# Performance work log

Measured on AMD Instinct MI355X. Metric: run time of the kernel, lower is better.

Reference implementation:

```python
import jax, jax.numpy as jnp
import numpy as np

B, T, C_IN = 64, 2048, 44
D = 512                      # d_model
DC = D // 2 + D // 2 + D // 4  # combined_dim = 640
RED = DC // 4                # SE reduction dim = 160
EPS = 1e-5


def setup_inputs() -> dict:
    key = jax.random.key(0)
    ks = iter(jax.random.split(key, 32))
    def w(shape, scale=None):
        s = scale if scale is not None else 1.0 / np.sqrt(shape[0])
        return jax.random.uniform(next(ks), shape, jnp.float32, -s, s)
    return {
        "x": jax.random.normal(next(ks), (B, T, C_IN), jnp.float32),
        # grouped projections (weights stored [in, out])
        "hw1": w((14, D // 2)), "hb1": w((D // 2,), 1.0 / np.sqrt(14)),
        "hw2": w((D // 2, D // 2)), "hb2": w((D // 2,)),
        "lw1": w((22, D // 2)), "lb1": w((D // 2,), 1.0 / np.sqrt(22)),
        "lw2": w((D // 2, D // 2)), "lb2": w((D // 2,)),
        "ew1": w((8, D // 4)), "eb1": w((D // 4,), 1.0 / np.sqrt(8)),
        "ew2": w((D // 4, D // 4)), "eb2": w((D // 4,)),
        # SE block (no bias)
        "se_w1": w((DC, RED)), "se_w2": w((RED, DC)),
        # SymmetryGate
        "gw": w((DC, DC)), "gb": w((DC,)),
        "pw": w((DC, DC)), "pb": w((DC,)),
        "ln_w": jnp.ones((DC,), jnp.float32), "ln_b": jnp.zeros((DC,), jnp.float32),
        # output proj + GroupNorm(8, D)
        "ow": w((DC, D)), "ob": w((DC,))[:D] if DC >= D else w((D,)),
        "gn_w": jnp.ones((D,), jnp.float32), "gn_b": jnp.zeros((D,), jnp.float32),
    }


def reference(x, hw1, hb1, hw2, hb2, lw1, lb1, lw2, lb2, ew1, eb1, ew2, eb2,
              se_w1, se_w2, gw, gb, pw, pb, ln_w, ln_b, ow, ob, gn_w, gn_b):
    silu = jax.nn.silu
    # grouped projections on channel slices (scale=2 -> 14/22/8)
    z_h = silu(x[..., :14] @ hw1 + hb1) @ hw2 + hb2        # [B,T,D/2]
    z_l = silu(x[..., 14:36] @ lw1 + lb1) @ lw2 + lb2      # [B,T,D/2]
    z_e = silu(x[..., 36:44] @ ew1 + eb1) @ ew2 + eb2      # [B,T,D/4]
    z = jnp.concatenate([z_h, z_l, z_e], axis=-1)          # [B,T,DC]
    # SE block: global time-average pooling then channel gating
    y_avg = z.mean(axis=1)                                  # [B,DC]
    se = jax.nn.sigmoid(jax.nn.relu(y_avg @ se_w1) @ se_w2) # [B,DC]
    z_se = z * se[:, None, :]
    # SymmetryGate (GLU + LayerNorm)
    g = jax.nn.sigmoid(z_se @ gw + gb)
    p = z_se @ pw + pb
    h = g * p + (1.0 - g) * z_se
    mu = h.mean(axis=-1, keepdims=True)
    var = h.var(axis=-1, keepdims=True)
    h = (h - mu) * jax.lax.rsqrt(var + EPS) * ln_w + ln_b
    # output projection
    out = h @ ow + ob                                       # [B,T,D]
    # GroupNorm(8, D) over channels (PyTorch normalizes per (group, T))
    G = 8
    og = out.reshape(B, T, G, D // G)
    m = og.mean(axis=(1, 3), keepdims=True)
    v = og.var(axis=(1, 3), keepdims=True)
    og = (og - m) * jax.lax.rsqrt(v + EPS)
    out = og.reshape(B, T, D) * gn_w + gn_b
    return out
```

## Files before the change

### kernel.cpp

```cpp
#include <hip/hip_runtime.h>
#include <hip/hip_bf16.h>
#include <cstdint>

#define B_   64
#define T_   2048
#define CIN  44
#define D_   512
#define DCC  640
#define REDD 160
#define BT   131072
#define EPSV 1e-5f

typedef __attribute__((ext_vector_type(8))) short short8;
typedef __attribute__((ext_vector_type(4))) float f32x4;

#define MFMA16(a,b,c) __builtin_amdgcn_mfma_f32_16x16x32_bf16(a,b,c,0,0,0)

__device__ __forceinline__ float bf2f(unsigned short u) {
    union { unsigned int i; float f; } v; v.i = ((unsigned int)u) << 16; return v.f;
}
__device__ __forceinline__ unsigned short f2bf(float f) {
    union { float f; unsigned int i; } v; v.f = f;
    unsigned int r = v.i + 0x7FFFu + ((v.i >> 16) & 1u);
    return (unsigned short)(r >> 16);
}

__global__ void kprep(const float* __restrict__ hw1, const float* __restrict__ lw1, const float* __restrict__ ew1,
                      const float* __restrict__ hb1, const float* __restrict__ lb1, const float* __restrict__ eb1,
                      const float* __restrict__ hw2, const float* __restrict__ lw2, const float* __restrict__ ew2,
                      const float* __restrict__ hb2, const float* __restrict__ lb2, const float* __restrict__ eb2,
                      const float* __restrict__ gw,  const float* __restrict__ pw,  const float* __restrict__ ow,
                      unsigned short* __restrict__ w1T, float* __restrict__ b1,
                      unsigned short* __restrict__ w2T, float* __restrict__ b2,
                      unsigned short* __restrict__ gwT, unsigned short* __restrict__ pwT,
                      unsigned short* __restrict__ owT)
{
    int tid = blockIdx.x * blockDim.x + threadIdx.x;
    int nth = gridDim.x * blockDim.x;
    for (int i = tid; i < 640 * 640; i += nth) {
        int c  = i / 40960, r = i - c * 40960;
        int kb = r / 2048;  int r2 = r - kb * 2048;
        int t  = r2 >> 9;   int l8 = r2 & 511;
        int lane = l8 >> 3, j = l8 & 7;
        int lid = lane & 15, quad = lane >> 4;
        int n = c * 64 + t * 16 + lid;
        int k = kb * 32 + quad * 8 + j;
        gwT[i] = f2bf(gw[(size_t)k * 640 + n]);
        pwT[i] = f2bf(pw[(size_t)k * 640 + n]);
    }
    for (int i = tid; i < 512 * 640; i += nth) {
        int c  = i / 40960, r = i - c * 40960;
        int kb = r / 2048;  int r2 = r - kb * 2048;
        int t  = r2 >> 9;   int l8 = r2 & 511;
        int lane = l8 >> 3, j = l8 & 7;
        int lid = lane & 15, quad = lane >> 4;
        int n = c * 64 + t * 16 + lid;
        int k = kb * 32 + quad * 8 + j;
        owT[i] = f2bf(ow[(size_t)k * 512 + n]);
    }
    for (int i = tid; i < 640 * 256; i += nth) {
        int c  = i / 16384, r = i - c * 16384;
        int kb = r / 2048;  int r2 = r - kb * 2048;
        int t  = r2 >> 9;   int l8 = r2 & 511;
        int lane = l8 >> 3, j = l8 & 7;
        int lid = lane & 15, quad = lane >> 4;
        int n = c * 64 + t * 16 + lid;
        int k = kb * 32 + quad * 8 + j;
        float v;
        if (n < 256)      v = hw2[k * 256 + n];
        else if (n < 512) v = lw2[k * 256 + (n - 256)];
        else              v = (k < 128) ? ew2[k * 128 + (n - 512)] : 0.0f;
        w2T[i] = f2bf(v);
    }
    for (int i = tid; i < 640 * 32; i += nth) {
        int ct = i >> 9;  int l8 = i & 511;
        int lane = l8 >> 3, j = l8 & 7;
        int lid = lane & 15, quad = lane >> 4;
        int n = ct * 16 + lid;
        int k = quad * 8 + j;
        float v = 0.0f;
        if (n < 256)      { if (k < 14) v = hw1[k * 256 + n]; }
        else if (n < 512) { if (k < 22) v = lw1[k * 256 + (n - 256)]; }
        else              { if (k < 8)  v = ew1[k * 128 + (n - 512)]; }
        w1T[i] = f2bf(v);
    }
    for (int i = tid; i < 640; i += nth) {
        b1[i] = (i < 256) ? hb1[i] : ((i < 512) ? lb1[i - 256] : eb1[i - 512]);
        b2[i] = (i < 256) ? hb2[i] : ((i < 512) ? lb2[i - 256] : eb2[i - 512]);
    }
}

#define ZSTEP(KB, CUR, NXT) { \
    const int kk = (KB) * 32; \
    short8 ah0 = *(const short8*)&su[(0*16 + lid) * 648 + kk + quad * 8]; \
    short8 ah1 = *(const short8*)&su[(1*16 + lid) * 648 + kk + quad * 8]; \
    short8 ah2 = *(const short8*)&su[(2*16 + lid) * 648 + kk + quad * 8]; \
    short8 ah3 = *(const short8*)&su[(3*16 + lid) * 648 + kk + quad * 8]; \
    short8 al0 = *(const short8*)&su[(0*16 + lid) * 648 + 256 + kk + quad * 8]; \
    short8 al1 = *(const short8*)&su[(1*16 + lid) * 648 + 256 + kk + quad * 8]; \
    short8 al2 = *(const short8*)&su[(2*16 + lid) * 648 + 256 + kk + quad * 8]; \
    short8 al3 = *(const short8*)&su[(3*16 + lid) * 648 + 256 + kk + quad * 8]; \
    if ((KB) + 1 < 8) { \
        NXT[0] = *(const short8*)(w2T + off[0] + ((KB) + 1) * 2048); \
        NXT[1] = *(const short8*)(w2T + off[1] + ((KB) + 1) * 2048); \
        NXT[2] = *(const short8*)(w2T + off[2] + ((KB) + 1) * 2048); \
        NXT[3] = *(const short8*)(w2T + off[3] + ((KB) + 1) * 2048); \
        if ((KB) + 1 < 4) NXT[4] = *(const short8*)(w2T + off[4] + ((KB) + 1) * 2048); \
    } \
    acc[0][0] = MFMA16(ah0, CUR[0], acc[0][0]); acc[0][1] = MFMA16(ah1, CUR[0], acc[0][1]); \
    acc[0][2] = MFMA16(ah2, CUR[0], acc[0][2]); acc[0][3] = MFMA16(ah3, CUR[0], acc[0][3]); \
    acc[1][0] = MFMA16(ah0, CUR[1], acc[1][0]); acc[1][1] = MFMA16(ah1, CUR[1], acc[1][1]); \
    acc[1][2] = MFMA16(ah2, CUR[1], acc[1][2]); acc[1][3] = MFMA16(ah3, CUR[1], acc[1][3]); \
    acc[2][0] = MFMA16(al0, CUR[2], acc[2][0]); acc[2][1] = MFMA16(al1, CUR[2], acc[2][1]); \
    acc[2][2] = MFMA16(al2, CUR[2], acc[2][2]); acc[2][3] = MFMA16(al3, CUR[2], acc[2][3]); \
    acc[3][0] = MFMA16(al0, CUR[3], acc[3][0]); acc[3][1] = MFMA16(al1, CUR[3], acc[3][1]); \
    acc[3][2] = MFMA16(al2, CUR[3], acc[3][2]); acc[3][3] = MFMA16(al3, CUR[3], acc[3][3]); \
    if ((KB) < 4) { \
        short8 ae0 = *(const short8*)&su[(0*16 + lid) * 648 + 512 + kk + quad * 8]; \
        short8 ae1 = *(const short8*)&su[(1*16 + lid) * 648 + 512 + kk + quad * 8]; \
        short8 ae2 = *(const short8*)&su[(2*16 + lid) * 648 + 512 + kk + quad * 8]; \
        short8 ae3 = *(const short8*)&su[(3*16 + lid) * 648 + 512 + kk + quad * 8]; \
        acc[4][0] = MFMA16(ae0, CUR[4], acc[4][0]); acc[4][1] = MFMA16(ae1, CUR[4], acc[4][1]); \
        acc[4][2] = MFMA16(ae2, CUR[4], acc[4][2]); acc[4][3] = MFMA16(ae3, CUR[4], acc[4][3]); \
    } }

__global__ __launch_bounds__(512) void k_z(const float* __restrict__ x,
                                           const unsigned short* __restrict__ w1T,
                                           const float* __restrict__ b1,
                                           const unsigned short* __restrict__ w2T,
                                           const float* __restrict__ b2,
                                           unsigned short* __restrict__ z,
                                           float* __restrict__ y_sum)
{
    __shared__ __align__(16) unsigned short sx[64 * 96];
    __shared__ __align__(16) unsigned short su[64 * 648];
    int m0 = blockIdx.x * 64;
    int bidx = m0 >> 11;
    const float* xsrc = x + (size_t)m0 * CIN;
    for (int i = threadIdx.x; i < 64 * 96; i += 512) {
        int r = i / 96, c = i - r * 96;
        int slab = c >> 5, kc = c & 31;
        float v = 0.0f;
        if (slab == 0)      { if (kc < 14) v = xsrc[r * CIN + kc]; }
        else if (slab == 1) { if (kc < 22) v = xsrc[r * CIN + 14 + kc]; }
        else                { if (kc < 8)  v = xsrc[r * CIN + 36 + kc]; }
        sx[i] = f2bf(v);
    }
    __syncthreads();
    int wave = threadIdx.x >> 6, lane = threadIdx.x & 63, lid = lane & 15, quad = lane >> 4;
    const f32x4 z4 = {0.f, 0.f, 0.f, 0.f};
    #pragma unroll
    for (int i = 0; i < 5; i++) {
        int ct = wave + 8 * i;
        int slab = ct >> 4;
        short8 bfr = *(const short8*)(w1T + (size_t)ct * 512 + lane * 8);
        int col = ct * 16 + lid;
        float bias = b1[col];
        #pragma unroll
        for (int rf = 0; rf < 4; rf++) {
            short8 a = *(const short8*)&sx[(rf * 16 + lid) * 96 + slab * 32 + quad * 8];
            f32x4 u = MFMA16(a, bfr, z4);
            #pragma unroll
            for (int r = 0; r < 4; r++) {
                float v0 = u[r] + bias;
                su[(rf * 16 + quad * 4 + r) * 648 + col] = f2bf(v0 / (1.0f + __expf(-v0)));
            }
        }
    }
    __syncthreads();
    int off[5];
    #pragma unroll
    for (int i = 0; i < 5; i++) {
        int ct = wave + 8 * i;
        off[i] = ((ct >> 2) * 32 + (ct & 3)) * 512 + lane * 8;
    }
    f32x4 acc[5][4];
    #pragma unroll
    for (int i = 0; i < 5; i++) { acc[i][0] = z4; acc[i][1] = z4; acc[i][2] = z4; acc[i][3] = z4; }
    short8 bA[5], bB[5];
    #pragma unroll
    for (int i = 0; i < 5; i++) bA[i] = *(const short8*)(w2T + off[i]);
    ZSTEP(0, bA, bB) ZSTEP(1, bB, bA) ZSTEP(2, bA, bB) ZSTEP(3, bB, bA)
    ZSTEP(4, bA, bB) ZSTEP(5, bB, bA) ZSTEP(6, bA, bB) ZSTEP(7, bB, bA)
    #pragma unroll
    for (int i = 0; i < 5; i++) {
        int ct = wave + 8 * i;
        int col = ct * 16 + lid;
        float bias = b2[col];
        float colsum = 0.0f;
        #pragma unroll
        for (int rf = 0; rf < 4; rf++) {
            #pragma unroll
            for (int r = 0; r < 4; r++) {
                float zv = acc[i][rf][r] + bias;
                z[(size_t)(m0 + rf * 16 + quad * 4 + r) * 640 + col] = f2bf(zv);
                colsum += zv;
            }
        }
        colsum += __shfl_xor(colsum, 16);
        colsum += __shfl_xor(colsum, 32);
        if (quad == 0) atomicAdd(&y_sum[bidx * 640 + col], colsum);
    }
}

__global__ void k_se(const float* __restrict__ y_sum, const float* __restrict__ se_w1,
                     const float* __restrict__ se_w2, float* __restrict__ se)
{
    __shared__ float ya[640];
    __shared__ float rr[160];
    int b = blockIdx.x;
    for (int i = threadIdx.x; i < 640; i += 256) ya[i] = y_sum[b * 640 + i] * (1.0f / 2048.0f);
    __syncthreads();
    for (int o = threadIdx.x; o < 160; o += 256) {
        float a = 0.f;
        for (int k = 0; k < 640; k++) a += ya[k] * se_w1[k * 160 + o];
        rr[o] = fmaxf(a, 0.f);
    }
    __syncthreads();
    for (int c = threadIdx.x; c < 640; c += 256) {
        float a = 0.f;
        for (int o = 0; o < 160; o++) a += rr[o] * se_w2[o * 640 + c];
        se[b * 640 + c] = 1.0f / (1.0f + __expf(-a));
    }
}

__global__ __launch_bounds__(512) void k_glu(const unsigned short* __restrict__ z,
                                             const float* __restrict__ se,
                                             const unsigned short* __restrict__ gwT,
                                             const unsigned short* __restrict__ pwT,
                                             const float* __restrict__ gb, const float* __restrict__ pb,
                                             unsigned short* __restrict__ h, float* __restrict__ hstats)
{
    __shared__ __align__(16) unsigned short sz[64 * 648];
    int m0 = blockIdx.x * 64;
    int bidx = m0 >> 11;
    const unsigned short* zsrc = z + (size_t)m0 * 640;
    const float* seb = se + bidx * 640;
    for (int i = threadIdx.x; i < 5120; i += 512) {
        int e = i * 8, r = e / 640, c = e - r * 640;
        short8 v = *(const short8*)(zsrc + e);
        unsigned short o8[8];
        #pragma unroll
        for (int j = 0; j < 8; j++) {
            float f = bf2f(((const unsigned short*)&v)[j]) * seb[c + j];
            o8[j] = f2bf(f);
        }
        *(short8*)&sz[r * 648 + c] = *(short8*)o8;
    }
    __syncthreads();
    int wave = threadIdx.x >> 6, lane = threadIdx.x & 63, lid = lane & 15, quad = lane >> 4;
    const f32x4 z4 = {0.f, 0.f, 0.f, 0.f};
    int off[5];
    #pragma unroll
    for (int i = 0; i < 5; i++) {
        int ct = wave + 8 * i;
        off[i] = ((ct >> 2) * 80 + (ct & 3)) * 512 + lane * 8;
    }
    f32x4 ag[5][4], ap[5][4];
    #pragma unroll
    for (int i = 0; i < 5; i++) {
        ag[i][0] = z4; ag[i][1] = z4; ag[i][2] = z4; ag[i][3] = z4;
        ap[i][0] = z4; ap[i][1] = z4; ap[i][2] = z4; ap[i][3] = z4;
    }
    short8 gbuf[5], pbuf[5];
    #pragma unroll
    for (int i = 0; i < 5; i++) gbuf[i] = *(const short8*)(gwT + off[i]);
    for (int kb = 0; kb < 20; kb++) {
        int kk = kb * 32;
        short8 a0 = *(const short8*)&sz[(0 * 16 + lid) * 648 + kk + quad * 8];
        short8 a1 = *(const short8*)&sz[(1 * 16 + lid) * 648 + kk + quad * 8];
        short8 a2 = *(const short8*)&sz[(2 * 16 + lid) * 648 + kk + quad * 8];
        short8 a3 = *(const short8*)&sz[(3 * 16 + lid) * 648 + kk + quad * 8];
        #pragma unroll
        for (int i = 0; i < 5; i++) pbuf[i] = *(const short8*)(pwT + off[i] + kk * 64);
        #pragma unroll
        for (int i = 0; i < 5; i++) {
            ag[i][0] = MFMA16(a0, gbuf[i], ag[i][0]);
            ag[i][1] = MFMA16(a1, gbuf[i], ag[i][1]);
            ag[i][2] = MFMA16(a2, gbuf[i], ag[i][2]);
            ag[i][3] = MFMA16(a3, gbuf[i], ag[i][3]);
        }
        if (kb < 19) {
            #pragma unroll
            for (int i = 0; i < 5; i++) gbuf[i] = *(const short8*)(gwT + off[i] + kk * 64 + 2048);
        }
        #pragma unroll
        for (int i = 0; i < 5; i++) {
            ap[i][0] = MFMA16(a0, pbuf[i], ap[i][0]);
            ap[i][1] = MFMA16(a1, pbuf[i], ap[i][1]);
            ap[i][2] = MFMA16(a2, pbuf[i], ap[i][2]);
            ap[i][3] = MFMA16(a3, pbuf[i], ap[i][3]);
        }
    }
    float hs[4][4] = {{0,0,0,0},{0,0,0,0},{0,0,0,0},{0,0,0,0}};
    float hq[4][4] = {{0,0,0,0},{0,0,0,0},{0,0,0,0},{0,0,0,0}};
    #pragma unroll
    for (int i = 0; i < 5; i++) {
        int ct = wave + 8 * i;
        int col = ct * 16 + lid;
        float gbv = gb[col], pbv = pb[col];
        #pragma unroll
        for (int rf = 0; rf < 4; rf++) {
            #pragma unroll
            for (int r = 0; r < 4; r++) {
                int row = rf * 16 + quad * 4 + r;
                float gl = ag[i][rf][r] + gbv;
                float pl = ap[i][rf][r] + pbv;
                float sg = 1.0f / (1.0f + __expf(-gl));
                float zv = bf2f(sz[row * 648 + col]);
                float hv = sg * pl + (1.0f - sg) * zv;
                h[(size_t)(m0 + row) * 640 + col] = f2bf(hv);
                hs[rf][r] += hv; hq[rf][r] += hv * hv;
            }
        }
    }
    #pragma unroll
    for (int s = 1; s < 16; s <<= 1) {
        #pragma unroll
        for (int rf = 0; rf < 4; rf++)
            #pragma unroll
            for (int r = 0; r < 4; r++) {
                hs[rf][r] += __shfl_xor(hs[rf][r], s);
                hq[rf][r] += __shfl_xor(hq[rf][r], s);
            }
    }
    if (lid == 0) {
        #pragma unroll
        for (int rf = 0; rf < 4; rf++)
            #pragma unroll
            for (int r = 0; r < 4; r++) {
                int row = m0 + rf * 16 + quad * 4 + r;
                atomicAdd(&hstats[row * 2 + 0], hs[rf][r]);
                atomicAdd(&hstats[row * 2 + 1], hq[rf][r]);
            }
    }
}

#define OSTEP(KB, CUR, NXT) { \
    const int kk = (KB) * 32; \
    short8 a0 = *(const short8*)&sh[(0 * 16 + lid) * 648 + kk + quad * 8]; \
    short8 a1 = *(const short8*)&sh[(1 * 16 + lid) * 648 + kk + quad * 8]; \
    short8 a2 = *(const short8*)&sh[(2 * 16 + lid) * 648 + kk + quad * 8]; \
    short8 a3 = *(const short8*)&sh[(3 * 16 + lid) * 648 + kk + quad * 8]; \
    if ((KB) < 19) { \
        NXT[0] = *(const short8*)(owT + off[0] + ((KB) + 1) * 2048); \
        NXT[1] = *(const short8*)(owT + off[1] + ((KB) + 1) * 2048); \
        NXT[2] = *(const short8*)(owT + off[2] + ((KB) + 1) * 2048); \
        NXT[3] = *(const short8*)(owT + off[3] + ((KB) + 1) * 2048); \
    } \
    acc[0][0] = MFMA16(a0, CUR[0], acc[0][0]); acc[0][1] = MFMA16(a1, CUR[0], acc[0][1]); \
    acc[0][2] = MFMA16(a2, CUR[0], acc[0][2]); acc[0][3] = MFMA16(a3, CUR[0], acc[0][3]); \
    acc[1][0] = MFMA16(a0, CUR[1], acc[1][0]); acc[1][1] = MFMA16(a1, CUR[1], acc[1][1]); \
    acc[1][2] = MFMA16(a2, CUR[1], acc[1][2]); acc[1][3] = MFMA16(a3, CUR[1], acc[1][3]); \
    acc[2][0] = MFMA16(a0, CUR[2], acc[2][0]); acc[2][1] = MFMA16(a1, CUR[2], acc[2][1]); \
    acc[2][2] = MFMA16(a2, CUR[2], acc[2][2]); acc[2][3] = MFMA16(a3, CUR[2], acc[2][3]); \
    acc[3][0] = MFMA16(a0, CUR[3], acc[3][0]); acc[3][1] = MFMA16(a1, CUR[3], acc[3][1]); \
    acc[3][2] = MFMA16(a2, CUR[3], acc[3][2]); acc[3][3] = MFMA16(a3, CUR[3], acc[3][3]); }

__global__ __launch_bounds__(512) void k_out(const unsigned short* __restrict__ h,
                                             const float* __restrict__ hstats,
                                             const float* __restrict__ ln_w, const float* __restrict__ ln_b,
                                             const unsigned short* __restrict__ owT,
                                             const float* __restrict__ ob,
                                             float* __restrict__ outp, float* __restrict__ gnstats)
{
    __shared__ __align__(16) unsigned short sh[64 * 648];
    __shared__ float sA[64], sB[64];
    int m0 = blockIdx.x * 64;
    int bidx = m0 >> 11;
    if (threadIdx.x < 64) {
        float s1 = hstats[(m0 + threadIdx.x) * 2 + 0];
        float s2 = hstats[(m0 + threadIdx.x) * 2 + 1];
        float mu = s1 * (1.0f / 640.0f);
        float var = s2 * (1.0f / 640.0f) - mu * mu;
        float rs = rsqrtf(var + EPSV);
        sA[threadIdx.x] = rs;
        sB[threadIdx.x] = -mu * rs;
    }
    __syncthreads();
    const unsigned short* hsrc = h + (size_t)m0 * 640;
    for (int i = threadIdx.x; i < 5120; i += 512) {
        int e = i * 8, r = e / 640, c = e - r * 640;
        short8 v = *(const short8*)(hsrc + e);
        float a = sA[r], bb = sB[r];
        unsigned short o8[8];
        #pragma unroll
        for (int j = 0; j < 8; j++) {
            float f = bf2f(((const unsigned short*)&v)[j]);
            f = f * a + bb;
            f = f * ln_w[c + j] + ln_b[c + j];
            o8[j] = f2bf(f);
        }
        *(short8*)&sh[r * 648 + c] = *(short8*)o8;
    }
    __syncthreads();
    int wave = threadIdx.x >> 6, lane = threadIdx.x & 63, lid = lane & 15, quad = lane >> 4;
    const f32x4 z4 = {0.f, 0.f, 0.f, 0.f};
    int off[4];
    #pragma unroll
    for (int i = 0; i < 4; i++) {
        int ct = wave + 8 * i;
        off[i] = ((ct >> 2) * 80 + (ct & 3)) * 512 + lane * 8;
    }
    f32x4 acc[4][4];
    #pragma unroll
    for (int i = 0; i < 4; i++) {
        acc[i][0] = z4; acc[i][1] = z4; acc[i][2] = z4; acc[i][3] = z4;
    }
    short8 bA[4], bB[4];
    #pragma unroll
    for (int i = 0; i < 4; i++) bA[i] = *(const short8*)(owT + off[i]);
    OSTEP(0, bA, bB)  OSTEP(1, bB, bA)  OSTEP(2, bA, bB)  OSTEP(3, bB, bA)
    OSTEP(4, bA, bB)  OSTEP(5, bB, bA)  OSTEP(6, bA, bB)  OSTEP(7, bB, bA)
    OSTEP(8, bA, bB)  OSTEP(9, bB, bA)  OSTEP(10, bA, bB) OSTEP(11, bB, bA)
    OSTEP(12, bA, bB) OSTEP(13, bB, bA) OSTEP(14, bA, bB) OSTEP(15, bB, bA)
    OSTEP(16, bA, bB) OSTEP(17, bB, bA) OSTEP(18, bA, bB) OSTEP(19, bB, bA)
    #pragma unroll
    for (int i = 0; i < 4; i++) {
        int ct = wave + 8 * i;
        int col = ct * 16 + lid;
        float obv = ob[col];
        float gs = 0.f, gq = 0.f;
        #pragma unroll
        for (int rf = 0; rf < 4; rf++) {
            #pragma unroll
            for (int r = 0; r < 4; r++) {
                int row = rf * 16 + quad * 4 + r;
                float v = acc[i][rf][r] + obv;
                outp[(size_t)(m0 + row) * 512 + col] = v;
                gs += v; gq += v * v;
            }
        }
        #pragma unroll
        for (int s = 1; s < 64; s <<= 1) { gs += __shfl_xor(gs, s); gq += __shfl_xor(gq, s); }
        if (lane == 0) {
            int grp = ct >> 2;
            atomicAdd(&gnstats[(bidx * 8 + grp) * 2 + 0], gs);
            atomicAdd(&gnstats[(bidx * 8 + grp) * 2 + 1], gq);
        }
    }
}

__global__ void k_gn(float* __restrict__ outp, const float* __restrict__ gnstats,
                     const float* __restrict__ gn_w, const float* __restrict__ gn_b)
{
    int idx = blockIdx.x * 256 + threadIdx.x;
    size_t e = (size_t)idx * 4;
    int c = (int)(e & 511);
    size_t row = e >> 9;
    int b = (int)(row >> 11);
    int grp = c >> 6;
    float s1 = gnstats[(b * 8 + grp) * 2 + 0];
    float s2 = gnstats[(b * 8 + grp) * 2 + 1];
    const float inv = 1.0f / 131072.0f;
    float mu = s1 * inv;
    float var = s2 * inv - mu * mu;
    float rs = rsqrtf(var + EPSV);
    float4 v = *(const float4*)(outp + e);
    float4 w = *(const float4*)(gn_w + c);
    float4 bb = *(const float4*)(gn_b + c);
    float4 o;
    o.x = (v.x - mu) * rs * w.x + bb.x;
    o.y = (v.y - mu) * rs * w.y + bb.y;
    o.z = (v.z - mu) * rs * w.z + bb.z;
    o.w = (v.w - mu) * rs * w.w + bb.w;
    *(float4*)(outp + e) = o;
}

extern "C" void kernel_launch(void* const* d_in, const int* in_sizes, int n_in,
                              void* d_out, int out_size, void* d_ws, size_t ws_size,
                              hipStream_t stream)
{
    const float* x     = (const float*)d_in[0];
    const float* hw1   = (const float*)d_in[1];
    const float* hb1   = (const float*)d_in[2];
    const float* hw2   = (const float*)d_in[3];
    const float* hb2   = (const float*)d_in[4];
    const float* lw1   = (const float*)d_in[5];
    const float* lb1   = (const float*)d_in[6];
    const float* lw2   = (const float*)d_in[7];
    const float* lb2   = (const float*)d_in[8];
    const float* ew1   = (const float*)d_in[9];
    const float* eb1   = (const float*)d_in[10];
    const float* ew2   = (const float*)d_in[11];
    const float* eb2   = (const float*)d_in[12];
    const float* se_w1 = (const float*)d_in[13];
    const float* se_w2 = (const float*)d_in[14];
    const float* gw    = (const float*)d_in[15];
    const float* gb    = (const float*)d_in[16];
    const float* pw    = (const float*)d_in[17];
    const float* pb    = (const float*)d_in[18];
    const float* ln_w  = (const float*)d_in[19];
    const float* ln_b  = (const float*)d_in[20];
    const float* ow    = (const float*)d_in[21];
    const float* ob    = (const float*)d_in[22];
    const float* gn_w  = (const float*)d_in[23];
    const float* gn_b  = (const float*)d_in[24];

    char* ws = (char*)d_ws;
    size_t off = 0;
    unsigned short* w2T  = (unsigned short*)(ws + off); off += (size_t)640 * 256 * 2;
    float*          b2   = (float*)(ws + off);          off += 640 * 4;
    unsigned short* gwT  = (unsigned short*)(ws + off); off += (size_t)640 * 640 * 2;
    unsigned short* pwT  = (unsigned short*)(ws + off); off += (size_t)640 * 640 * 2;
    unsigned short* owT  = (unsigned short*)(ws + off); off += (size_t)512 * 640 * 2;
    unsigned short* w1T  = (unsigned short*)(ws + off); off += (size_t)640 * 32 * 2;
    float*          b1   = (float*)(ws + off);          off += 640 * 4;
    float*          ysum = (float*)(ws + off);          off += (size_t)64 * 640 * 4;
    float*          sebuf= (float*)(ws + off);          off += (size_t)64 * 640 * 4;
    float*          hstat= (float*)(ws + off);          off += (size_t)BT * 2 * 4;
    float*          gnst = (float*)(ws + off);          off += (size_t)64 * 8 * 2 * 4;
    unsigned short* hbuf = (unsigned short*)(ws + off); off += (size_t)BT * 640 * 2;

    unsigned short* zbuf = (unsigned short*)d_out;
    float*          outp = (float*)d_out;

    hipMemsetAsync(ysum, 0, (size_t)64 * 640 * 4, stream);
    hipMemsetAsync(hstat, 0, (size_t)BT * 2 * 4, stream);
    hipMemsetAsync(gnst, 0, (size_t)64 * 8 * 2 * 4, stream);

    kprep<<<512, 256, 0, stream>>>(hw1, lw1, ew1, hb1, lb1, eb1,
                                   hw2, lw2, ew2, hb2, lb2, eb2,
                                   gw, pw, ow, w1T, b1, w2T, b2, gwT, pwT, owT);
    k_z<<<BT / 64, 512, 0, stream>>>(x, w1T, b1, w2T, b2, zbuf, ysum);
    k_se<<<64, 256, 0, stream>>>(ysum, se_w1, se_w2, sebuf);
    k_glu<<<BT / 64, 512, 0, stream>>>(zbuf, sebuf, gwT, pwT, gb, pb, hbuf, hstat);
    k_out<<<BT / 64, 512, 0, stream>>>(hbuf, hstat, ln_w, ln_b, owT, ob, outp, gnst);
    k_gn<<<(BT * 512) / (256 * 4), 256, 0, stream>>>(outp, gnst, gn_w, gn_b);
}
```

Baseline: 1.266 ms.

## Fuse GLU and output projection kernels, keeping h in registers and LDS

Merges k_glu and k_out into one kernel, so the gated result h stays in registers. LayerNorm statistics are reduced through shared memory instead of global atomics, and the normalized h is written back into the same LDS tile before the output GEMM. This removes the global h write and read and the hstat memset. The GLU GEMM also double-buffers both gate and projection weight fragments. In exchange, register pressure rises because the fused kernel holds 40 accumulators plus the double buffers, which may lower occupancy or cause spills. z now lives in the workspace rather than aliasing the output buffer.

```diff
diff --git a/kernel.cpp b/kernel.cpp
--- a/kernel.cpp
+++ b/kernel.cpp
@@ -224,129 +224,44 @@
     }
 }
 
-__global__ __launch_bounds__(512) void k_glu(const unsigned short* __restrict__ z,
-                                             const float* __restrict__ se,
-                                             const unsigned short* __restrict__ gwT,
-                                             const unsigned short* __restrict__ pwT,
-                                             const float* __restrict__ gb, const float* __restrict__ pb,
-                                             unsigned short* __restrict__ h, float* __restrict__ hstats)
-{
-    __shared__ __align__(16) unsigned short sz[64 * 648];
-    int m0 = blockIdx.x * 64;
-    int bidx = m0 >> 11;
-    const unsigned short* zsrc = z + (size_t)m0 * 640;
-    const float* seb = se + bidx * 640;
-    for (int i = threadIdx.x; i < 5120; i += 512) {
-        int e = i * 8, r = e / 640, c = e - r * 640;
-        short8 v = *(const short8*)(zsrc + e);
-        unsigned short o8[8];
-        #pragma unroll
-        for (int j = 0; j < 8; j++) {
-            float f = bf2f(((const unsigned short*)&v)[j]) * seb[c + j];
-            o8[j] = f2bf(f);
-        }
-        *(short8*)&sz[r * 648 + c] = *(short8*)o8;
-    }
-    __syncthreads();
-    int wave = threadIdx.x >> 6, lane = threadIdx.x & 63, lid = lane & 15, quad = lane >> 4;
-    const f32x4 z4 = {0.f, 0.f, 0.f, 0.f};
-    int off[5];
-    #pragma unroll
-    for (int i = 0; i < 5; i++) {
-        int ct = wave + 8 * i;
-        off[i] = ((ct >> 2) * 80 + (ct & 3)) * 512 + lane * 8;
-    }
-    f32x4 ag[5][4], ap[5][4];
-    #pragma unroll
-    for (int i = 0; i < 5; i++) {
-        ag[i][0] = z4; ag[i][1] = z4; ag[i][2] = z4; ag[i][3] = z4;
-        ap[i][0] = z4; ap[i][1] = z4; ap[i][2] = z4; ap[i][3] = z4;
-    }
-    short8 gbuf[5], pbuf[5];
-    #pragma unroll
-    for (int i = 0; i < 5; i++) gbuf[i] = *(const short8*)(gwT + off[i]);
-    for (int kb = 0; kb < 20; kb++) {
-        int kk = kb * 32;
-        short8 a0 = *(const short8*)&sz[(0 * 16 + lid) * 648 + kk + quad * 8];
-        short8 a1 = *(const short8*)&sz[(1 * 16 + lid) * 648 + kk + quad * 8];
-        short8 a2 = *(const short8*)&sz[(2 * 16 + lid) * 648 + kk + quad * 8];
-        short8 a3 = *(const short8*)&sz[(3 * 16 + lid) * 648 + kk + quad * 8];
-        #pragma unroll
-        for (int i = 0; i < 5; i++) pbuf[i] = *(const short8*)(pwT + off[i] + kk * 64);
-        #pragma unroll
-        for (int i = 0; i < 5; i++) {
-            ag[i][0] = MFMA16(a0, gbuf[i], ag[i][0]);
-            ag[i][1] = MFMA16(a1, gbuf[i], ag[i][1]);
-            ag[i][2] = MFMA16(a2, gbuf[i], ag[i][2]);
-            ag[i][3] = MFMA16(a3, gbuf[i], ag[i][3]);
-        }
-        if (kb < 19) {
-            #pragma unroll
-            for (int i = 0; i < 5; i++) gbuf[i] = *(const short8*)(gwT + off[i] + kk * 64 + 2048);
-        }
-        #pragma unroll
-        for (int i = 0; i < 5; i++) {
-            ap[i][0] = MFMA16(a0, pbuf[i], ap[i][0]);
-            ap[i][1] = MFMA16(a1, pbuf[i], ap[i][1]);
-            ap[i][2] = MFMA16(a2, pbuf[i], ap[i][2]);
-            ap[i][3] = MFMA16(a3, pbuf[i], ap[i][3]);
-        }
-    }
-    float hs[4][4] = {{0,0,0,0},{0,0,0,0},{0,0,0,0},{0,0,0,0}};
-    float hq[4][4] = {{0,0,0,0},{0,0,0,0},{0,0,0,0},{0,0,0,0}};
-    #pragma unroll
-    for (int i = 0; i < 5; i++) {
-        int ct = wave + 8 * i;
-        int col = ct * 16 + lid;
-        float gbv = gb[col], pbv = pb[col];
-        #pragma unroll
-        for (int rf = 0; rf < 4; rf++) {
-            #pragma unroll
-            for (int r = 0; r < 4; r++) {
-                int row = rf * 16 + quad * 4 + r;
-                float gl = ag[i][rf][r] + gbv;
-                float pl = ap[i][rf][r] + pbv;
-                float sg = 1.0f / (1.0f + __expf(-gl));
-                float zv = bf2f(sz[row * 648 + col]);
-                float hv = sg * pl + (1.0f - sg) * zv;
-                h[(size_t)(m0 + row) * 640 + col] = f2bf(hv);
-                hs[rf][r] += hv; hq[rf][r] += hv * hv;
-            }
-        }
-    }
-    #pragma unroll
-    for (int s = 1; s < 16; s <<= 1) {
-        #pragma unroll
-        for (int rf = 0; rf < 4; rf++)
-            #pragma unroll
-            for (int r = 0; r < 4; r++) {
-                hs[rf][r] += __shfl_xor(hs[rf][r], s);
-                hq[rf][r] += __shfl_xor(hq[rf][r], s);
-            }
-    }
-    if (lid == 0) {
-        #pragma unroll
-        for (int rf = 0; rf < 4; rf++)
-            #pragma unroll
-            for (int r = 0; r < 4; r++) {
-                int row = m0 + rf * 16 + quad * 4 + r;
-                atomicAdd(&hstats[row * 2 + 0], hs[rf][r]);
-                atomicAdd(&hstats[row * 2 + 1], hq[rf][r]);
-            }
-    }
-}
+#define GSTEP(KB, CG, CP, NG, NP) { \
+    const int kk = (KB) * 32; \
+    short8 a0 = *(const short8*)&sz[(0*16 + lid) * 648 + kk + quad * 8]; \
+    short8 a1 = *(const short8*)&sz[(1*16 + lid) * 648 + kk + quad * 8]; \
+    short8 a2 = *(const short8*)&sz[(2*16 + lid) * 648 + kk + quad * 8]; \
+    short8 a3 = *(const short8*)&sz[(3*16 + lid) * 648 + kk + quad * 8]; \
+    if ((KB) < 19) { \
+        _Pragma("unroll") \
+        for (int i = 0; i < 5; i++) { \
+            NG[i] = *(const short8*)(gwT + offG[i] + ((KB) + 1) * 2048); \
+            NP[i] = *(const short8*)(pwT + offG[i] + ((KB) + 1) * 2048); \
+        } \
+    } \
+    _Pragma("unroll") \
+    for (int i = 0; i < 5; i++) { \
+        ag[i][0] = MFMA16(a0, CG[i], ag[i][0]); \
+        ag[i][1] = MFMA16(a1, CG[i], ag[i][1]); \
+        ag[i][2] = MFMA16(a2, CG[i], ag[i][2]); \
+        ag[i][3] = MFMA16(a3, CG[i], ag[i][3]); \
+    } \
+    _Pragma("unroll") \
+    for (int i = 0; i < 5; i++) { \
+        ap[i][0] = MFMA16(a0, CP[i], ap[i][0]); \
+        ap[i][1] = MFMA16(a1, CP[i], ap[i][1]); \
+        ap[i][2] = MFMA16(a2, CP[i], ap[i][2]); \
+        ap[i][3] = MFMA16(a3, CP[i], ap[i][3]); \
+    } }
 
 #define OSTEP(KB, CUR, NXT) { \
     const int kk = (KB) * 32; \
-    short8 a0 = *(const short8*)&sh[(0 * 16 + lid) * 648 + kk + quad * 8]; \
-    short8 a1 = *(const short8*)&sh[(1 * 16 + lid) * 648 + kk + quad * 8]; \
-    short8 a2 = *(const short8*)&sh[(2 * 16 + lid) * 648 + kk + quad * 8]; \
-    short8 a3 = *(const short8*)&sh[(3 * 16 + lid) * 648 + kk + quad * 8]; \
+    short8 a0 = *(const short8*)&sz[(0 * 16 + lid) * 648 + kk + quad * 8]; \
+    short8 a1 = *(const short8*)&sz[(1 * 16 + lid) * 648 + kk + quad * 8]; \
+    short8 a2 = *(const short8*)&sz[(2 * 16 + lid) * 648 + kk + quad * 8]; \
+    short8 a3 = *(const short8*)&sz[(3 * 16 + lid) * 648 + kk + quad * 8]; \
     if ((KB) < 19) { \
-        NXT[0] = *(const short8*)(owT + off[0] + ((KB) + 1) * 2048); \
-        NXT[1] = *(const short8*)(owT + off[1] + ((KB) + 1) * 2048); \
-        NXT[2] = *(const short8*)(owT + off[2] + ((KB) + 1) * 2048); \
-        NXT[3] = *(const short8*)(owT + off[3] + ((KB) + 1) * 2048); \
+        _Pragma("unroll") \
+        for (int i = 0; i < 4; i++) \
+            NXT[i] = *(const short8*)(owT + offO[i] + ((KB) + 1) * 2048); \
     } \
     acc[0][0] = MFMA16(a0, CUR[0], acc[0][0]); acc[0][1] = MFMA16(a1, CUR[0], acc[0][1]); \
     acc[0][2] = MFMA16(a2, CUR[0], acc[0][2]); acc[0][3] = MFMA16(a3, CUR[0], acc[0][3]); \
@@ -357,20 +272,107 @@
     acc[3][0] = MFMA16(a0, CUR[3], acc[3][0]); acc[3][1] = MFMA16(a1, CUR[3], acc[3][1]); \
     acc[3][2] = MFMA16(a2, CUR[3], acc[3][2]); acc[3][3] = MFMA16(a3, CUR[3], acc[3][3]); }
 
-__global__ __launch_bounds__(512) void k_out(const unsigned short* __restrict__ h,
-                                             const float* __restrict__ hstats,
-                                             const float* __restrict__ ln_w, const float* __restrict__ ln_b,
-                                             const unsigned short* __restrict__ owT,
-                                             const float* __restrict__ ob,
-                                             float* __restrict__ outp, float* __restrict__ gnstats)
+__global__ __launch_bounds__(512) void k_gluout(const unsigned short* __restrict__ z,
+                                                const float* __restrict__ se,
+                                                const unsigned short* __restrict__ gwT,
+                                                const unsigned short* __restrict__ pwT,
+                                                const float* __restrict__ gb, const float* __restrict__ pb,
+                                                const float* __restrict__ ln_w, const float* __restrict__ ln_b,
+                                                const unsigned short* __restrict__ owT,
+                                                const float* __restrict__ ob,
+                                                float* __restrict__ outp, float* __restrict__ gnstats)
 {
-    __shared__ __align__(16) unsigned short sh[64 * 648];
+    __shared__ __align__(16) unsigned short sz[64 * 648];
+    __shared__ float spart[64][8];
+    __shared__ float sqart[64][8];
     __shared__ float sA[64], sB[64];
     int m0 = blockIdx.x * 64;
     int bidx = m0 >> 11;
+    const unsigned short* zsrc = z + (size_t)m0 * 640;
+    const float* seb = se + bidx * 640;
+    for (int i = threadIdx.x; i < 5120; i += 512) {
+        int e = i * 8, r = e / 640, c = e - r * 640;
+        short8 v = *(const short8*)(zsrc + e);
+        unsigned short o8[8];
+        #pragma unroll
+        for (int j = 0; j < 8; j++) {
+            float f = bf2f(((const unsigned short*)&v)[j]) * seb[c + j];
+            o8[j] = f2bf(f);
+        }
+        *(short8*)&sz[r * 648 + c] = *(short8*)o8;
+    }
+    __syncthreads();
+    int wave = threadIdx.x >> 6, lane = threadIdx.x & 63, lid = lane & 15, quad = lane >> 4;
+    const f32x4 z4 = {0.f, 0.f, 0.f, 0.f};
+    int offG[5];
+    #pragma unroll
+    for (int i = 0; i < 5; i++) {
+        int ct = wave + 8 * i;
+        offG[i] = ((ct >> 2) * 80 + (ct & 3)) * 512 + lane * 8;
+    }
+    f32x4 ag[5][4], ap[5][4];
+    #pragma unroll
+    for (int i = 0; i < 5; i++) {
+        ag[i][0] = z4; ag[i][1] = z4; ag[i][2] = z4; ag[i][3] = z4;
+        ap[i][0] = z4; ap[i][1] = z4; ap[i][2] = z4; ap[i][3] = z4;
+    }
+    short8 gA[5], gB[5], pA[5], pB[5];
+    #pragma unroll
+    for (int i = 0; i < 5; i++) {
+        gA[i] = *(const short8*)(gwT + offG[i]);
+        pA[i] = *(const short8*)(pwT + offG[i]);
+    }
+    for (int kb = 0; kb < 20; kb += 2) {
+        GSTEP(kb, gA, pA, gB, pB)
+        GSTEP(kb + 1, gB, pB, gA, pA)
+    }
+    float hs[4][4] = {{0,0,0,0},{0,0,0,0},{0,0,0,0},{0,0,0,0}};
+    float hq[4][4] = {{0,0,0,0},{0,0,0,0},{0,0,0,0},{0,0,0,0}};
+    #pragma unroll
+    for (int i = 0; i < 5; i++) {
+        int ct = wave + 8 * i;
+        int col = ct * 16 + lid;
+        float gbv = gb[col], pbv = pb[col];
+        #pragma unroll
+        for (int rf = 0; rf < 4; rf++) {
+            #pragma unroll
+            for (int r = 0; r < 4; r++) {
+                int row = rf * 16 + quad * 4 + r;
+                float gl = ag[i][rf][r] + gbv;
+                float pl = ap[i][rf][r] + pbv;
+                float sg = 1.0f / (1.0f + __expf(-gl));
+                float zv = bf2f(sz[row * 648 + col]);
+                float hv = sg * pl + (1.0f - sg) * zv;
+                ag[i][rf][r] = hv;
+                hs[rf][r] += hv; hq[rf][r] += hv * hv;
+            }
+        }
+    }
+    #pragma unroll
+    for (int s = 1; s < 16; s <<= 1) {
+        #pragma unroll
+        for (int rf = 0; rf < 4; rf++)
+            #pragma unroll
+            for (int r = 0; r < 4; r++) {
+                hs[rf][r] += __shfl_xor(hs[rf][r], s);
+                hq[rf][r] += __shfl_xor(hq[rf][r], s);
+            }
+    }
+    if (lid == 0) {
+        #pragma unroll
+        for (int rf = 0; rf < 4; rf++)
+            #pragma unroll
+            for (int r = 0; r < 4; r++) {
+                int row = rf * 16 + quad * 4 + r;
+                spart[row][wave] = hs[rf][r];
+                sqart[row][wave] = hq[rf][r];
+            }
+    }
+    __syncthreads();
     if (threadIdx.x < 64) {
-        float s1 = hstats[(m0 + threadIdx.x) * 2 + 0];
-        float s2 = hstats[(m0 + threadIdx.x) * 2 + 1];
+        float s1 = 0.f, s2 = 0.f;
+        #pragma unroll
+        for (int w = 0; w < 8; w++) { s1 += spart[threadIdx.x][w]; s2 += sqart[threadIdx.x][w]; }
         float mu = s1 * (1.0f / 640.0f);
         float var = s2 * (1.0f / 640.0f) - mu * mu;
         float rs = rsqrtf(var + EPSV);
@@ -378,43 +380,38 @@
         sB[threadIdx.x] = -mu * rs;
     }
     __syncthreads();
-    const unsigned short* hsrc = h + (size_t)m0 * 640;
-    for (int i = threadIdx.x; i < 5120; i += 512) {
-        int e = i * 8, r = e / 640, c = e - r * 640;
-        short8 v = *(const short8*)(hsrc + e);
-        float a = sA[r], bb = sB[r];
-        unsigned short o8[8];
-        #pragma unroll
-        for (int j = 0; j < 8; j++) {
-            float f = bf2f(((const unsigned short*)&v)[j]);
-            f = f * a + bb;
-            f = f * ln_w[c + j] + ln_b[c + j];
-            o8[j] = f2bf(f);
-        }
-        *(short8*)&sh[r * 648 + c] = *(short8*)o8;
-    }
-    __syncthreads();
-    int wave = threadIdx.x >> 6, lane = threadIdx.x & 63, lid = lane & 15, quad = lane >> 4;
-    const f32x4 z4 = {0.f, 0.f, 0.f, 0.f};
-    int off[4];
+    #pragma unroll
+    for (int i = 0; i < 5; i++) {
+        int ct = wave + 8 * i;
+        int col = ct * 16 + lid;
+        float lw = ln_w[col], lb = ln_b[col];
+        #pragma unroll
+        for (int rf = 0; rf < 4; rf++) {
+            #pragma unroll
+            for (int r = 0; r < 4; r++) {
+                int row = rf * 16 + quad * 4 + r;
+                float f = ag[i][rf][r] * sA[row] + sB[row];
+                sz[row * 648 + col] = f2bf(f * lw + lb);
+            }
+        }
+    }
+    __syncthreads();
+    int offO[4];
     #pragma unroll
     for (int i = 0; i < 4; i++) {
         int ct = wave + 8 * i;
-        off[i] = ((ct >> 2) * 80 + (ct & 3)) * 512 + lane * 8;
+        offO[i] = ((ct >> 2) * 80 + (ct & 3)) * 512 + lane * 8;
     }
     f32x4 acc[4][4];
     #pragma unroll
-    for (int i = 0; i < 4; i++) {
-        acc[i][0] = z4; acc[i][1] = z4; acc[i][2] = z4; acc[i][3] = z4;
-    }
+    for (int i = 0; i < 4; i++) { acc[i][0] = z4; acc[i][1] = z4; acc[i][2] = z4; acc[i][3] = z4; }
     short8 bA[4], bB[4];
     #pragma unroll
-    for (int i = 0; i < 4; i++) bA[i] = *(const short8*)(owT + off[i]);
-    OSTEP(0, bA, bB)  OSTEP(1, bB, bA)  OSTEP(2, bA, bB)  OSTEP(3, bB, bA)
-    OSTEP(4, bA, bB)  OSTEP(5, bB, bA)  OSTEP(6, bA, bB)  OSTEP(7, bB, bA)
-    OSTEP(8, bA, bB)  OSTEP(9, bB, bA)  OSTEP(10, bA, bB) OSTEP(11, bB, bA)
-    OSTEP(12, bA, bB) OSTEP(13, bB, bA) OSTEP(14, bA, bB) OSTEP(15, bB, bA)
-    OSTEP(16, bA, bB) OSTEP(17, bB, bA) OSTEP(18, bA, bB) OSTEP(19, bB, bA)
+    for (int i = 0; i < 4; i++) bA[i] = *(const short8*)(owT + offO[i]);
+    for (int kb = 0; kb < 20; kb += 2) {
+        OSTEP(kb, bA, bB)
+        OSTEP(kb + 1, bB, bA)
+    }
     #pragma unroll
     for (int i = 0; i < 4; i++) {
         int ct = wave + 8 * i;
@@ -508,15 +505,12 @@
     float*          b1   = (float*)(ws + off);          off += 640 * 4;
     float*          ysum = (float*)(ws + off);          off += (size_t)64 * 640 * 4;
     float*          sebuf= (float*)(ws + off);          off += (size_t)64 * 640 * 4;
-    float*          hstat= (float*)(ws + off);          off += (size_t)BT * 2 * 4;
     float*          gnst = (float*)(ws + off);          off += (size_t)64 * 8 * 2 * 4;
-    unsigned short* hbuf = (unsigned short*)(ws + off); off += (size_t)BT * 640 * 2;
-
-    unsigned short* zbuf = (unsigned short*)d_out;
-    float*          outp = (float*)d_out;
+    unsigned short* zbuf = (unsigned short*)(ws + off); off += (size_t)BT * 640 * 2;
+
+    float* outp = (float*)d_out;
 
     hipMemsetAsync(ysum, 0, (size_t)64 * 640 * 4, stream);
-    hipMemsetAsync(hstat, 0, (size_t)BT * 2 * 4, stream);
     hipMemsetAsync(gnst, 0, (size_t)64 * 8 * 2 * 4, stream);
 
     kprep<<<512, 256, 0, stream>>>(hw1, lw1, ew1, hb1, lb1, eb1,
@@ -524,7 +518,7 @@
                                    gw, pw, ow, w1T, b1, w2T, b2, gwT, pwT, owT);
     k_z<<<BT / 64, 512, 0, stream>>>(x, w1T, b1, w2T, b2, zbuf, ysum);
     k_se<<<64, 256, 0, stream>>>(ysum, se_w1, se_w2, sebuf);
-    k_glu<<<BT / 64, 512, 0, stream>>>(zbuf, sebuf, gwT, pwT, gb, pb, hbuf, hstat);
-    k_out<<<BT / 64, 512, 0, stream>>>(hbuf, hstat, ln_w, ln_b, owT, ob, outp, gnst);
+    k_gluout<<<BT / 64, 512, 0, stream>>>(zbuf, sebuf, gwT, pwT, gb, pb,
+                                          ln_w, ln_b, owT, ob, outp, gnst);
     k_gn<<<(BT * 512) / (256 * 4), 256, 0, stream>>>(outp, gnst, gn_w, gn_b);
 }
```

Result: slower. 1.514 ms (+19.5%).
